# Kernel tuning notes

Hardware: AMD Instinct MI355X
Metric: run time of the kernel (lower is better)

Reference implementation:

```python
import jax, jax.numpy as jnp
import numpy as np

N, IN1, IN2, OUT, DX, DY = 32, 4, 4, 128, 128, 128


def setup_inputs() -> dict:
    key = jax.random.key(0)
    k = jax.random.split(key, 6)
    x = jax.random.normal(k[0], (N, IN1, DX), dtype=jnp.float32)
    y = jax.random.normal(k[1], (N, IN2, DY), dtype=jnp.float32)
    # kernel_C: [out_channels, in1*in2]
    C = jax.random.normal(k[2], (OUT, IN1 * IN2), dtype=jnp.float32) * 0.1
    # one Conv1d pair (kernel_size=3 -> only j=1: k=2, dilation=2, padding=1)
    W_A = jax.random.normal(k[3], (OUT, IN1 * IN2, 2), dtype=jnp.float32) * 0.1
    W_B = jax.random.normal(k[4], (OUT, IN1 * IN2, 2), dtype=jnp.float32) * 0.1
    bias = jax.random.uniform(k[5], (OUT,), dtype=jnp.float32, minval=-0.5, maxval=0.5)
    return {"x": x, "y": y, "C": C, "W_A": W_A, "W_B": W_B, "bias": bias}


def _dilated_conv(inp, w):
    # PyTorch Conv1d(kernel_size=2, stride=1, padding=1, dilation=2, bias=False)
    return jax.lax.conv_general_dilated(
        inp, w, window_strides=(1,), padding=[(1, 1)], rhs_dilation=(2,),
        dimension_numbers=("NCH", "OIH", "NCH"))


def reference(x, y, C, W_A, W_B, bias):
    n, in1, dx = x.shape
    _, in2, dy = y.shape
    out_ch = C.shape[0]
    # batch_cross_product: channel c = c1*in2 + c2 of outer product, then einsum with C.
    # Fused form (same math, no [N, in1*dx, in2*dy] intermediate):
    Cr = C.reshape(out_ch, in1, in2)
    bcp = jnp.einsum("nci,ndj,ocd->noij", x, y, Cr)  # [N, out, dx, dy]
    # x.repeat(1, in2, 1) / y.repeat(1, in1, 1) == tile along channel dim
    xA = jnp.tile(x, (1, in2, 1))  # [N, in1*in2, dx]
    yB = jnp.tile(y, (1, in1, 1))  # [N, in1*in2, dy]
    a = _dilated_conv(xA, W_A)  # [N, out, dx]
    b = _dilated_conv(yB, W_B)  # [N, out, dy]
    out = bcp + a[:, :, :, None] + b[:, :, None, :]
    return out + bias[None, :, None, None]
```

## Files before the change

kernel.cpp:

```cpp
#include <hip/hip_runtime.h>


__global__ __launch_bounds__(256) void scvc_kernel(
    const float* __restrict__ x,
    const float* __restrict__ y,
    const float* __restrict__ C,
    const float* __restrict__ WA,
    const float* __restrict__ WB,
    const float* __restrict__ bias,
    float* __restrict__ out)
{
    const int n   = blockIdx.x >> 6;
    const int og  = blockIdx.x & 63;
    const int o0  = og << 1;
    const int tid = threadIdx.x;

    __shared__ float csh[2][16];
    __shared__ float wash[2][8];
    __shared__ float wbsh[2][8];
    __shared__ float t4[2][128][4];
    __shared__ float arow[2][128];
    __shared__ float bcol[2][128];

    const float* xb = x + n * 512;
    const float* yb = y + n * 512;

    if (tid < 64) {
        const int oi = tid >> 5;
        const int o  = o0 + oi;
        const int t  = tid & 31;
        if (t < 16) {
            csh[oi][t] = C[o * 16 + t];
        } else if (t < 24) {
            const int idx = t - 16;
            const int c = idx >> 1, k = idx & 1;
            float s = 0.f;
            #pragma unroll
            for (int r = 0; r < 4; ++r) s += WA[o * 32 + (4 * r + c) * 2 + k];
            wash[oi][idx] = s;
        } else {
            const int idx = t - 24;
            const int c = idx >> 1, k = idx & 1;
            float s = 0.f;
            #pragma unroll
            for (int r = 0; r < 4; ++r) s += WB[o * 32 + (4 * r + c) * 2 + k];
            wbsh[oi][idx] = s;
        }
    }
    __syncthreads();

    if (tid < 128) {
        const int i = tid;
        float xv[4], xm[4], xp[4];
        #pragma unroll
        for (int c = 0; c < 4; ++c) {
            xv[c] = xb[c * 128 + i];
            xm[c] = (i > 0)   ? xb[c * 128 + i - 1] : 0.f;
            xp[c] = (i < 127) ? xb[c * 128 + i + 1] : 0.f;
        }
        #pragma unroll
        for (int oi = 0; oi < 2; ++oi) {
            #pragma unroll
            for (int d = 0; d < 4; ++d) {
                float s = 0.f;
                #pragma unroll
                for (int c = 0; c < 4; ++c) s += xv[c] * csh[oi][c * 4 + d];
                t4[oi][i][d] = s;
            }
            float a = 0.f;
            #pragma unroll
            for (int c = 0; c < 4; ++c)
                a += xm[c] * wash[oi][c * 2] + xp[c] * wash[oi][c * 2 + 1];
            arow[oi][i] = a;
        }
    } else {
        const int j = tid - 128;
        float ym[4], yp[4];
        #pragma unroll
        for (int c = 0; c < 4; ++c) {
            ym[c] = (j > 0)   ? yb[c * 128 + j - 1] : 0.f;
            yp[c] = (j < 127) ? yb[c * 128 + j + 1] : 0.f;
        }
        #pragma unroll
        for (int oi = 0; oi < 2; ++oi) {
            float b = bias[o0 + oi];
            #pragma unroll
            for (int c = 0; c < 4; ++c)
                b += ym[c] * wbsh[oi][c * 2] + yp[c] * wbsh[oi][c * 2 + 1];
            bcol[oi][j] = b;
        }
    }
    __syncthreads();

    const int wave = tid >> 6;
    const int lane = tid & 63;
    const int col4 = (lane & 31) * 4;
    const int half = lane >> 5;

    float yr[4][4];
    #pragma unroll
    for (int d = 0; d < 4; ++d) {
        const float4 v = *(const float4*)(yb + d * 128 + col4);
        yr[d][0] = v.x; yr[d][1] = v.y; yr[d][2] = v.z; yr[d][3] = v.w;
    }

    #pragma unroll
    for (int oi = 0; oi < 2; ++oi) {
        const float4 bv = *(const float4*)(&bcol[oi][col4]);
        float bj[4];
        bj[0] = bv.x; bj[1] = bv.y; bj[2] = bv.z; bj[3] = bv.w;

        float* op = out + (((long)(n * 128 + o0 + oi)) << 14) + col4;
        #pragma unroll
        for (int it = 0; it < 16; ++it) {
            const int i = wave * 32 + it * 2 + half;
            const float4 t = *(const float4*)(&t4[oi][i][0]);
            const float ai = arow[oi][i];
            float4 r;
            r.x = t.x * yr[0][0] + t.y * yr[1][0] + t.z * yr[2][0] + t.w * yr[3][0] + (ai + bj[0]);
            r.y = t.x * yr[0][1] + t.y * yr[1][1] + t.z * yr[2][1] + t.w * yr[3][1] + (ai + bj[1]);
            r.z = t.x * yr[0][2] + t.y * yr[1][2] + t.z * yr[2][2] + t.w * yr[3][2] + (ai + bj[2]);
            r.w = t.x * yr[0][3] + t.y * yr[1][3] + t.z * yr[2][3] + t.w * yr[3][3] + (ai + bj[3]);
            *(float4*)(op + i * 128) = r;
        }
    }
}

extern "C" void kernel_launch(void* const* d_in, const int* in_sizes, int n_in,
                              void* d_out, int out_size, void* d_ws, size_t ws_size,
                              hipStream_t stream) {
    const float* x    = (const float*)d_in[0];
    const float* y    = (const float*)d_in[1];
    const float* C    = (const float*)d_in[2];
    const float* WA   = (const float*)d_in[3];
    const float* WB   = (const float*)d_in[4];
    const float* bias = (const float*)d_in[5];
    float* out = (float*)d_out;

    scvc_kernel<<<32 * 64, 256, 0, stream>>>(x, y, C, WA, WB, bias, out);
}
```

Before: 263.1 us.

## Process eight output channels per block to amortize per-block setup

Each block now covers 8 output channels in four passes of 2 instead of a single pair, and the grid shrinks from 2048 to 512 blocks. Weight preloading for all 8 channels and the x/y neighbour and y-row register loads happen once per block and are reused across the passes. The cost is two extra barriers per pass and fewer blocks to spread across the compute units, which reduces parallelism for a kernel bound by output stores.

Result: slower. 299.3 us (+13.8%).

```diff
diff --git a/kernel.cpp b/kernel.cpp
--- a/kernel.cpp
+++ b/kernel.cpp
@@ -10,14 +10,14 @@
     const float* __restrict__ bias,
     float* __restrict__ out)
 {
-    const int n   = blockIdx.x >> 6;
-    const int og  = blockIdx.x & 63;
-    const int o0  = og << 1;
-    const int tid = threadIdx.x;
+    const int n     = blockIdx.x >> 4;
+    const int chunk = blockIdx.x & 15;
+    const int tid   = threadIdx.x;
+    const int obase = chunk * 8;
 
-    __shared__ float csh[2][16];
-    __shared__ float wash[2][8];
-    __shared__ float wbsh[2][8];
+    __shared__ float csh8[8][16];
+    __shared__ float wash8[8][8];
+    __shared__ float wbsh8[8][8];
     __shared__ float t4[2][128][4];
     __shared__ float arow[2][128];
     __shared__ float bcol[2][128];
@@ -25,78 +25,50 @@
     const float* xb = x + n * 512;
     const float* yb = y + n * 512;
 
-    if (tid < 64) {
-        const int oi = tid >> 5;
-        const int o  = o0 + oi;
-        const int t  = tid & 31;
-        if (t < 16) {
-            csh[oi][t] = C[o * 16 + t];
-        } else if (t < 24) {
-            const int idx = t - 16;
-            const int c = idx >> 1, k = idx & 1;
-            float s = 0.f;
-            #pragma unroll
-            for (int r = 0; r < 4; ++r) s += WA[o * 32 + (4 * r + c) * 2 + k];
-            wash[oi][idx] = s;
-        } else {
-            const int idx = t - 24;
-            const int c = idx >> 1, k = idx & 1;
-            float s = 0.f;
-            #pragma unroll
-            for (int r = 0; r < 4; ++r) s += WB[o * 32 + (4 * r + c) * 2 + k];
-            wbsh[oi][idx] = s;
-        }
+    if (tid < 128) {
+        const int oo = tid >> 4, t = tid & 15;
+        csh8[oo][t] = C[(obase + oo) * 16 + t];
+    } else if (tid < 192) {
+        const int idx = tid - 128;
+        const int oo = idx >> 3, w = idx & 7;
+        const int c = w >> 1, k = w & 1;
+        float s = 0.f;
+        #pragma unroll
+        for (int r = 0; r < 4; ++r) s += WA[(obase + oo) * 32 + (4 * r + c) * 2 + k];
+        wash8[oo][w] = s;
+    } else {
+        const int idx = tid - 192;
+        const int oo = idx >> 3, w = idx & 7;
+        const int c = w >> 1, k = w & 1;
+        float s = 0.f;
+        #pragma unroll
+        for (int r = 0; r < 4; ++r) s += WB[(obase + oo) * 32 + (4 * r + c) * 2 + k];
+        wbsh8[oo][w] = s;
     }
-    __syncthreads();
 
+    float xv[4], xm[4], xp[4];
+    float ymv[4], ypv[4];
     if (tid < 128) {
         const int i = tid;
-        float xv[4], xm[4], xp[4];
         #pragma unroll
         for (int c = 0; c < 4; ++c) {
             xv[c] = xb[c * 128 + i];
             xm[c] = (i > 0)   ? xb[c * 128 + i - 1] : 0.f;
             xp[c] = (i < 127) ? xb[c * 128 + i + 1] : 0.f;
         }
-        #pragma unroll
-        for (int oi = 0; oi < 2; ++oi) {
-            #pragma unroll
-            for (int d = 0; d < 4; ++d) {
-                float s = 0.f;
-                #pragma unroll
-                for (int c = 0; c < 4; ++c) s += xv[c] * csh[oi][c * 4 + d];
-                t4[oi][i][d] = s;
-            }
-            float a = 0.f;
-            #pragma unroll
-            for (int c = 0; c < 4; ++c)
-                a += xm[c] * wash[oi][c * 2] + xp[c] * wash[oi][c * 2 + 1];
-            arow[oi][i] = a;
-        }
     } else {
         const int j = tid - 128;
-        float ym[4], yp[4];
         #pragma unroll
         for (int c = 0; c < 4; ++c) {
-            ym[c] = (j > 0)   ? yb[c * 128 + j - 1] : 0.f;
-            yp[c] = (j < 127) ? yb[c * 128 + j + 1] : 0.f;
-        }
-        #pragma unroll
-        for (int oi = 0; oi < 2; ++oi) {
-            float b = bias[o0 + oi];
-            #pragma unroll
-            for (int c = 0; c < 4; ++c)
-                b += ym[c] * wbsh[oi][c * 2] + yp[c] * wbsh[oi][c * 2 + 1];
-            bcol[oi][j] = b;
+            ymv[c] = (j > 0)   ? yb[c * 128 + j - 1] : 0.f;
+            ypv[c] = (j < 127) ? yb[c * 128 + j + 1] : 0.f;
         }
     }
-    __syncthreads();
 
     const int wave = tid >> 6;
     const int lane = tid & 63;
     const int col4 = (lane & 31) * 4;
     const int half = lane >> 5;
-
     float yr[4][4];
     #pragma unroll
     for (int d = 0; d < 4; ++d) {
@@ -104,24 +76,64 @@
         yr[d][0] = v.x; yr[d][1] = v.y; yr[d][2] = v.z; yr[d][3] = v.w;
     }
 
-    #pragma unroll
-    for (int oi = 0; oi < 2; ++oi) {
-        const float4 bv = *(const float4*)(&bcol[oi][col4]);
-        float bj[4];
-        bj[0] = bv.x; bj[1] = bv.y; bj[2] = bv.z; bj[3] = bv.w;
+    __syncthreads();
 
-        float* op = out + (((long)(n * 128 + o0 + oi)) << 14) + col4;
+    for (int p = 0; p < 4; ++p) {
+        if (p) __syncthreads();
+
+        const int o0 = obase + 2 * p;
+
+        if (tid < 128) {
+            const int i = tid;
+            #pragma unroll
+            for (int oi = 0; oi < 2; ++oi) {
+                const int oo = 2 * p + oi;
+                #pragma unroll
+                for (int d = 0; d < 4; ++d) {
+                    float s = 0.f;
+                    #pragma unroll
+                    for (int c = 0; c < 4; ++c) s += xv[c] * csh8[oo][c * 4 + d];
+                    t4[oi][i][d] = s;
+                }
+                float a = 0.f;
+                #pragma unroll
+                for (int c = 0; c < 4; ++c)
+                    a += xm[c] * wash8[oo][c * 2] + xp[c] * wash8[oo][c * 2 + 1];
+                arow[oi][i] = a;
+            }
+        } else {
+            const int j = tid - 128;
+            #pragma unroll
+            for (int oi = 0; oi < 2; ++oi) {
+                const int oo = 2 * p + oi;
+                float b = bias[o0 + oi];
+                #pragma unroll
+                for (int c = 0; c < 4; ++c)
+                    b += ymv[c] * wbsh8[oo][c * 2] + ypv[c] * wbsh8[oo][c * 2 + 1];
+                bcol[oi][j] = b;
+            }
+        }
+        __syncthreads();
+
         #pragma unroll
-        for (int it = 0; it < 16; ++it) {
-            const int i = wave * 32 + it * 2 + half;
-            const float4 t = *(const float4*)(&t4[oi][i][0]);
-            const float ai = arow[oi][i];
-            float4 r;
-            r.x = t.x * yr[0][0] + t.y * yr[1][0] + t.z * yr[2][0] + t.w * yr[3][0] + (ai + bj[0]);
-            r.y = t.x * yr[0][1] + t.y * yr[1][1] + t.z * yr[2][1] + t.w * yr[3][1] + (ai + bj[1]);
-            r.z = t.x * yr[0][2] + t.y * yr[1][2] + t.z * yr[2][2] + t.w * yr[3][2] + (ai + bj[2]);
-            r.w = t.x * yr[0][3] + t.y * yr[1][3] + t.z * yr[2][3] + t.w * yr[3][3] + (ai + bj[3]);
-            *(float4*)(op + i * 128) = r;
+        for (int oi = 0; oi < 2; ++oi) {
+            const float4 bv = *(const float4*)(&bcol[oi][col4]);
+            float bj[4];
+            bj[0] = bv.x; bj[1] = bv.y; bj[2] = bv.z; bj[3] = bv.w;
+
+            float* op = out + (((long)(n * 128 + o0 + oi)) << 14) + col4;
+            #pragma unroll
+            for (int it = 0; it < 16; ++it) {
+                const int i = wave * 32 + it * 2 + half;
+                const float4 t = *(const float4*)(&t4[oi][i][0]);
+                const float ai = arow[oi][i];
+                float4 r;
+                r.x = t.x * yr[0][0] + t.y * yr[1][0] + t.z * yr[2][0] + t.w * yr[3][0] + (ai + bj[0]);
+                r.y = t.x * yr[0][1] + t.y * yr[1][1] + t.z * yr[2][1] + t.w * yr[3][1] + (ai + bj[1]);
+                r.z = t.x * yr[0][2] + t.y * yr[1][2] + t.z * yr[2][2] + t.w * yr[3][2] + (ai + bj[2]);
+                r.w = t.x * yr[0][3] + t.y * yr[1][3] + t.z * yr[2][3] + t.w * yr[3][3] + (ai + bj[3]);
+                *(float4*)(op + i * 128) = r;
+            }
         }
     }
 }
@@ -137,5 +149,5 @@
     const float* bias = (const float*)d_in[5];
     float* out = (float*)d_out;
 
-    scvc_kernel<<<32 * 64, 256, 0, stream>>>(x, y, C, WA, WB, bias, out);
+    scvc_kernel<<<32 * 16, 256, 0, stream>>>(x, y, C, WA, WB, bias, out);
 }
```
